# Kernel optimization log

Hardware: AMD Instinct MI355X
Metric: run time of the kernel (lower is better)

The kernel has to match this reference:

```python
import jax, jax.numpy as jnp
import numpy as np

N, D_IN, D_OUT = 8192, 1024, 1024

def setup_inputs() -> dict:
    key = jax.random.key(0)
    kx, kq, kk, kv = jax.random.split(key, 4)
    s = 1.0 / np.sqrt(D_IN)
    return {
        "x": jax.random.normal(kx, (N, D_IN), dtype=jnp.float32),
        "Wq": jax.random.uniform(kq, (D_OUT, D_IN), dtype=jnp.float32, minval=-s, maxval=s),
        "Wk": jax.random.uniform(kk, (D_OUT, D_IN), dtype=jnp.float32, minval=-s, maxval=s),
        "Wv": jax.random.uniform(kv, (D_OUT, D_IN), dtype=jnp.float32, minval=-s, maxval=s),
    }

def reference(x, Wq, Wk, Wv):
    # Linear layers: y = x @ W.T (no bias, qkv_bias=False)
    q = x @ Wq.T  # [N, d_out]
    k = x @ Wk.T
    v = x @ Wv.T
    scores = q @ k.T  # [N, N]
    weights = jax.nn.softmax(scores / jnp.sqrt(jnp.float32(k.shape[-1])), axis=-1)
    return weights @ v  # [N, d_out]
```

## Files before the change

### kernel.cpp

```cpp
#include <hip/hip_runtime.h>
#include <stdint.h>

typedef __bf16 bf16_t;
typedef __bf16 bf16x8 __attribute__((ext_vector_type(8)));
typedef float f32x4 __attribute__((ext_vector_type(4)));
typedef int i32x4 __attribute__((ext_vector_type(4)));
typedef int i32x8 __attribute__((ext_vector_type(8)));

typedef const __attribute__((address_space(1))) void gv_t;
typedef __attribute__((address_space(3))) void lv_t;


template <int LDK>
__device__ __forceinline__ void stage_half2(const bf16_t* g, bf16_t* lh,
                                            int wave, int lane) {
#pragma unroll
  for (int i = 0; i < 2; ++i) {
    const int ub = i * 8192 + wave * 1024;
    const int o = ub + lane * 16;
    const int row = o >> 7;
    const int kb = (o & 127) ^ ((row & 7) << 4);
    const char* src = (const char*)g + (size_t)row * (LDK * 2) + kb;
    __builtin_amdgcn_global_load_lds((gv_t*)src, (lv_t*)(lh + (ub >> 1)), 16, 0, 0);
  }
}

__device__ __forceinline__ bf16x8 ld_frag2(const bf16_t* h, int r, int s, int lane) {
  int byte = r * 128 + s * 64 + ((lane >> 4) << 4);
  byte ^= (r & 7) << 4;
  return *(const bf16x8*)((const char*)h + byte);
}

template <int NN, int KEXT, int LDK>
__global__ __launch_bounds__(512) void gemm8p(
    const bf16_t* __restrict__ A, const bf16_t* __restrict__ Bt,
    float* __restrict__ Cf0, bf16_t* __restrict__ Cf1b,
    const float* __restrict__ rvec) {
  __shared__ __align__(16) bf16_t L[2][4][8192];

  const int tid = threadIdx.x;
  const int wave = tid >> 6;
  const int lane = tid & 63;

  const int bid = blockIdx.x;
  const int x = bid & 7;
  const int j = bid >> 3;
  const int ks = j >> 4;
  const int tm = (x << 2) | (j & 3);
  const int tn = (j >> 2) & 3;

  const bf16_t* Ab = A + (size_t)tm * (256 * LDK) + (size_t)ks * KEXT;
  const bf16_t* Bb = Bt + (size_t)tn * (256 * LDK) + (size_t)ks * KEXT;

  const int wr64 = (wave >> 2) * 64;
  const int wc32 = (wave & 3) * 32;
  const int fr = lane & 15;
  constexpr int nt = KEXT >> 6;

  f32x4 acc00[4][2], acc01[4][2], acc10[4][2], acc11[4][2];
#pragma unroll
  for (int m = 0; m < 4; ++m)
#pragma unroll
    for (int n = 0; n < 2; ++n) {
      acc00[m][n] = (f32x4){0.f, 0.f, 0.f, 0.f};
      acc01[m][n] = (f32x4){0.f, 0.f, 0.f, 0.f};
      acc10[m][n] = (f32x4){0.f, 0.f, 0.f, 0.f};
      acc11[m][n] = (f32x4){0.f, 0.f, 0.f, 0.f};
    }

  stage_half2<LDK>(Ab, &L[0][0][0], wave, lane);
  stage_half2<LDK>(Ab + (size_t)128 * LDK, &L[0][1][0], wave, lane);
  stage_half2<LDK>(Bb, &L[0][2][0], wave, lane);
  stage_half2<LDK>(Bb + (size_t)128 * LDK, &L[0][3][0], wave, lane);
  stage_half2<LDK>(Ab + 64, &L[1][0][0], wave, lane);
  stage_half2<LDK>(Bb + 64, &L[1][2][0], wave, lane);
  stage_half2<LDK>(Bb + (size_t)128 * LDK + 64, &L[1][3][0], wave, lane);
  asm volatile("s_waitcnt vmcnt(6)" ::: "memory");
  __builtin_amdgcn_s_barrier();

  bf16x8 a[4][2], bA[2][2], bB[2][2];

#pragma unroll 1
  for (int t = 0; t < nt; ++t) {
    const int cur = t & 1;
    const bf16_t* A0h = &L[cur][0][0];
    const bf16_t* A1h = &L[cur][1][0];
    const bf16_t* B0h = &L[cur][2][0];
    const bf16_t* B1h = &L[cur][3][0];

#pragma unroll
    for (int m = 0; m < 4; ++m)
#pragma unroll
      for (int s = 0; s < 2; ++s)
        a[m][s] = ld_frag2(A0h, wr64 + m * 16 + fr, s, lane);
#pragma unroll
    for (int n = 0; n < 2; ++n)
#pragma unroll
      for (int s = 0; s < 2; ++s)
        bA[n][s] = ld_frag2(B0h, wc32 + n * 16 + fr, s, lane);
    if (t + 1 < nt)
      stage_half2<LDK>(Ab + (size_t)128 * LDK + (t + 1) * 64, &L[cur ^ 1][1][0],
                       wave, lane);
    __builtin_amdgcn_s_barrier();
    __builtin_amdgcn_s_setprio(1);
#pragma unroll
    for (int s = 0; s < 2; ++s)
#pragma unroll
      for (int m = 0; m < 4; ++m)
#pragma unroll
        for (int n = 0; n < 2; ++n)
          acc00[m][n] = __builtin_amdgcn_mfma_f32_16x16x32_bf16(a[m][s], bA[n][s],
                                                                acc00[m][n], 0, 0, 0);
    __builtin_amdgcn_s_setprio(0);
    __builtin_amdgcn_s_barrier();

#pragma unroll
    for (int n = 0; n < 2; ++n)
#pragma unroll
      for (int s = 0; s < 2; ++s)
        bB[n][s] = ld_frag2(B1h, wc32 + n * 16 + fr, s, lane);
    if (t + 2 < nt)
      stage_half2<LDK>(Ab + (t + 2) * 64, &L[cur][0][0], wave, lane);
    __builtin_amdgcn_s_barrier();
    __builtin_amdgcn_s_setprio(1);
#pragma unroll
    for (int s = 0; s < 2; ++s)
#pragma unroll
      for (int m = 0; m < 4; ++m)
#pragma unroll
        for (int n = 0; n < 2; ++n)
          acc01[m][n] = __builtin_amdgcn_mfma_f32_16x16x32_bf16(a[m][s], bB[n][s],
                                                                acc01[m][n], 0, 0, 0);
    __builtin_amdgcn_s_setprio(0);
    __builtin_amdgcn_s_barrier();

#pragma unroll
    for (int m = 0; m < 4; ++m)
#pragma unroll
      for (int s = 0; s < 2; ++s)
        a[m][s] = ld_frag2(A1h, wr64 + m * 16 + fr, s, lane);
    if (t + 2 < nt)
      stage_half2<LDK>(Bb + (t + 2) * 64, &L[cur][2][0], wave, lane);
    __builtin_amdgcn_s_barrier();
    __builtin_amdgcn_s_setprio(1);
#pragma unroll
    for (int s = 0; s < 2; ++s)
#pragma unroll
      for (int m = 0; m < 4; ++m)
#pragma unroll
        for (int n = 0; n < 2; ++n)
          acc11[m][n] = __builtin_amdgcn_mfma_f32_16x16x32_bf16(a[m][s], bB[n][s],
                                                                acc11[m][n], 0, 0, 0);
    __builtin_amdgcn_s_setprio(0);
    __builtin_amdgcn_s_barrier();

    if (t + 2 < nt)
      stage_half2<LDK>(Bb + (size_t)128 * LDK + (t + 2) * 64, &L[cur][3][0],
                       wave, lane);
    __builtin_amdgcn_s_barrier();
    __builtin_amdgcn_s_setprio(1);
#pragma unroll
    for (int s = 0; s < 2; ++s)
#pragma unroll
      for (int m = 0; m < 4; ++m)
#pragma unroll
        for (int n = 0; n < 2; ++n)
          acc10[m][n] = __builtin_amdgcn_mfma_f32_16x16x32_bf16(a[m][s], bA[n][s],
                                                                acc10[m][n], 0, 0, 0);
    __builtin_amdgcn_s_setprio(0);
    if (t + 2 < nt)
      asm volatile("s_waitcnt vmcnt(6)" ::: "memory");
    else
      asm volatile("s_waitcnt vmcnt(0)" ::: "memory");
    __builtin_amdgcn_s_barrier();
  }

  const int fro = (lane >> 4) * 4;
#define STORE_QUAD(ACC, QM, QN)                                                  \
  _Pragma("unroll") for (int m = 0; m < 4; ++m) {                                \
    _Pragma("unroll") for (int n = 0; n < 2; ++n) {                              \
      const int row = tm * 256 + QM * 128 + wr64 + m * 16 + fro;                 \
      const int col = tn * 256 + QN * 128 + wc32 + n * 16 + fr;                  \
      const float4 rv = *(const float4*)&rvec[row];                              \
      if (ks == 0) {                                                             \
        _Pragma("unroll") for (int jj = 0; jj < 4; ++jj)                         \
            Cf0[(size_t)(row + jj) * NN + col] =                                 \
                ACC[m][n][jj] * ((const float*)&rv)[jj];                         \
      } else {                                                                   \
        _Pragma("unroll") for (int jj = 0; jj < 4; ++jj)                         \
            Cf1b[(size_t)(row + jj) * NN + col] =                                \
                (bf16_t)(ACC[m][n][jj] * ((const float*)&rv)[jj]);               \
      }                                                                          \
    }                                                                            \
  }
  STORE_QUAD(acc00, 0, 0)
  STORE_QUAD(acc01, 0, 1)
  STORE_QUAD(acc10, 1, 0)
  STORE_QUAD(acc11, 1, 1)
#undef STORE_QUAD
}

template <int NN, int KEXT, int LDK>
__global__ __launch_bounds__(512) void gemm2p(
    const bf16_t* __restrict__ A, const bf16_t* __restrict__ Bt,
    uint8_t* __restrict__ qo, uint8_t* __restrict__ ko,
    bf16_t* __restrict__ vtb) {
  __shared__ __align__(16) bf16_t L[2][3][8192];

  const int tid = threadIdx.x;
  const int wave = tid >> 6;
  const int lane = tid & 63;

  const int bid = blockIdx.x;
  const int x = bid & 7;
  const int j = bid >> 3;
  const int tm = (x << 2) | (j & 3);
  const int tn = j >> 2;

  const bf16_t* Ab = A + (size_t)tm * (256 * LDK);
  const bf16_t* Bb = Bt + (size_t)tn * (128 * LDK);

  const int wr64 = (wave >> 2) * 64;
  const int wc32 = (wave & 3) * 32;
  const int fr = lane & 15;
  constexpr int nt = KEXT >> 6;

  f32x4 acc0[4][2], acc1[4][2];
#pragma unroll
  for (int m = 0; m < 4; ++m)
#pragma unroll
    for (int n = 0; n < 2; ++n) {
      acc0[m][n] = (f32x4){0.f, 0.f, 0.f, 0.f};
      acc1[m][n] = (f32x4){0.f, 0.f, 0.f, 0.f};
    }

  stage_half2<LDK>(Ab, &L[0][0][0], wave, lane);
  stage_half2<LDK>(Ab + (size_t)128 * LDK, &L[0][1][0], wave, lane);
  stage_half2<LDK>(Bb, &L[0][2][0], wave, lane);
  stage_half2<LDK>(Ab + 64, &L[1][0][0], wave, lane);
  stage_half2<LDK>(Bb + 64, &L[1][2][0], wave, lane);
  asm volatile("s_waitcnt vmcnt(4)" ::: "memory");
  __builtin_amdgcn_s_barrier();

  bf16x8 a[4][2], b[2][2];

#pragma unroll 1
  for (int t = 0; t < nt; ++t) {
    const int cur = t & 1;
    const bf16_t* A0h = &L[cur][0][0];
    const bf16_t* A1h = &L[cur][1][0];
    const bf16_t* Bh = &L[cur][2][0];

#pragma unroll
    for (int m = 0; m < 4; ++m)
#pragma unroll
      for (int s = 0; s < 2; ++s)
        a[m][s] = ld_frag2(A0h, wr64 + m * 16 + fr, s, lane);
#pragma unroll
    for (int n = 0; n < 2; ++n)
#pragma unroll
      for (int s = 0; s < 2; ++s)
        b[n][s] = ld_frag2(Bh, wc32 + n * 16 + fr, s, lane);
    if (t + 1 < nt)
      stage_half2<LDK>(Ab + (size_t)128 * LDK + (t + 1) * 64, &L[cur ^ 1][1][0],
                       wave, lane);
    __builtin_amdgcn_s_barrier();
    __builtin_amdgcn_s_setprio(1);
#pragma unroll
    for (int s = 0; s < 2; ++s)
#pragma unroll
      for (int m = 0; m < 4; ++m)
#pragma unroll
        for (int n = 0; n < 2; ++n)
          acc0[m][n] = __builtin_amdgcn_mfma_f32_16x16x32_bf16(a[m][s], b[n][s],
                                                               acc0[m][n], 0, 0, 0);
    __builtin_amdgcn_s_setprio(0);
    __builtin_amdgcn_s_barrier();

#pragma unroll
    for (int m = 0; m < 4; ++m)
#pragma unroll
      for (int s = 0; s < 2; ++s)
        a[m][s] = ld_frag2(A1h, wr64 + m * 16 + fr, s, lane);
    if (t + 2 < nt) {
      stage_half2<LDK>(Ab + (t + 2) * 64, &L[cur][0][0], wave, lane);
      stage_half2<LDK>(Bb + (t + 2) * 64, &L[cur][2][0], wave, lane);
    }
    __builtin_amdgcn_s_barrier();
    __builtin_amdgcn_s_setprio(1);
#pragma unroll
    for (int s = 0; s < 2; ++s)
#pragma unroll
      for (int m = 0; m < 4; ++m)
#pragma unroll
        for (int n = 0; n < 2; ++n)
          acc1[m][n] = __builtin_amdgcn_mfma_f32_16x16x32_bf16(a[m][s], b[n][s],
                                                               acc1[m][n], 0, 0, 0);
    __builtin_amdgcn_s_setprio(0);
    if (t + 2 < nt)
      asm volatile("s_waitcnt vmcnt(4)" ::: "memory");
    else
      asm volatile("s_waitcnt vmcnt(0)" ::: "memory");
    __builtin_amdgcn_s_barrier();
  }

  const int fro = (lane >> 4) * 4;
#define STORE_HALF(ACC, QM)                                                      \
  _Pragma("unroll") for (int m = 0; m < 4; ++m) {                                \
    _Pragma("unroll") for (int n = 0; n < 2; ++n) {                              \
      const int row = tm * 256 + QM * 128 + wr64 + m * 16 + fro;                 \
      const int col = tn * 128 + wc32 + n * 16 + fr;                             \
      if (col < 1024) {                                                          \
        _Pragma("unroll") for (int jj = 0; jj < 4; ++jj) {                       \
          int pk = __builtin_amdgcn_cvt_pk_fp8_f32(ACC[m][n][jj],                \
                                                   ACC[m][n][jj], 0, false);     \
          qo[(size_t)(row + jj) * 1024 + col] = (uint8_t)pk;                     \
        }                                                                        \
      } else if (col < 2048) {                                                   \
        _Pragma("unroll") for (int jj = 0; jj < 4; ++jj) {                       \
          int pk = __builtin_amdgcn_cvt_pk_fp8_f32(ACC[m][n][jj],                \
                                                   ACC[m][n][jj], 0, false);     \
          ko[(size_t)(row + jj) * 1024 + (col - 1024)] = (uint8_t)pk;            \
        }                                                                        \
      } else {                                                                   \
        union { bf16_t h[4]; uint2 u; } tpk;                                     \
        _Pragma("unroll") for (int jj = 0; jj < 4; ++jj)                         \
            tpk.h[jj] = (bf16_t)ACC[m][n][jj];                                   \
        *(uint2*)&vtb[(size_t)(col - 2048) * 8192 + row] = tpk.u;                \
      }                                                                          \
    }                                                                            \
  }
  STORE_HALF(acc0, 0)
  STORE_HALF(acc1, 1)
#undef STORE_HALF
}


__device__ __forceinline__ void stage_half8(const uint8_t* g, uint8_t* lh,
                                            int wave, int lane) {
#pragma unroll
  for (int i = 0; i < 2; ++i) {
    const int ub = i * 8192 + wave * 1024;
    const int o = ub + lane * 16;
    const int row = o >> 7;
    const int col = (o & 127) ^ ((row & 7) << 4);
    __builtin_amdgcn_global_load_lds((gv_t*)(g + (size_t)row * 1024 + col),
                                     (lv_t*)(lh + ub), 16, 0, 0);
  }
}

__device__ __forceinline__ i32x8 ld_frag8h(const uint8_t* h, int r, int lane) {
  const int sw = (r & 7) << 4;
  const int kg = (lane >> 4) * 32;
  const uint8_t* b = h + r * 128;
  i32x4 lo = *(const i32x4*)(b + (kg ^ sw));
  i32x4 hi = *(const i32x4*)(b + ((kg ^ sw) ^ 16));
  i32x8 v;
  v[0] = lo[0]; v[1] = lo[1]; v[2] = lo[2]; v[3] = lo[3];
  v[4] = hi[0]; v[5] = hi[1]; v[6] = hi[2]; v[7] = hi[3];
  return v;
}

__global__ __launch_bounds__(512) void scores8p(
    const uint8_t* __restrict__ qf, const uint8_t* __restrict__ kf,
    bf16_t* __restrict__ S, float* __restrict__ partial) {
  __shared__ __align__(16) uint8_t L[2][4][16384];

  const int tid = threadIdx.x;
  const int wave = tid >> 6;
  const int lane = tid & 63;

  const int bid = blockIdx.x;
  const int x = bid & 7;
  const int j = bid >> 3;
  const int tm = (x << 2) | (j & 3);
  const int tn = j >> 2;

  const uint8_t* Ab = qf + (size_t)tm * 256 * 1024;
  const uint8_t* Bb = kf + (size_t)tn * 256 * 1024;

  const int wr64 = (wave >> 2) * 64;
  const int wc32 = (wave & 3) * 32;
  const int fr = lane & 15;
  constexpr int nt = 8;

  f32x4 acc00[4][2], acc01[4][2], acc10[4][2], acc11[4][2];
#pragma unroll
  for (int m = 0; m < 4; ++m)
#pragma unroll
    for (int n = 0; n < 2; ++n) {
      acc00[m][n] = (f32x4){0.f, 0.f, 0.f, 0.f};
      acc01[m][n] = (f32x4){0.f, 0.f, 0.f, 0.f};
      acc10[m][n] = (f32x4){0.f, 0.f, 0.f, 0.f};
      acc11[m][n] = (f32x4){0.f, 0.f, 0.f, 0.f};
    }

  stage_half8(Ab, &L[0][0][0], wave, lane);
  stage_half8(Ab + (size_t)128 * 1024, &L[0][1][0], wave, lane);
  stage_half8(Bb, &L[0][2][0], wave, lane);
  stage_half8(Bb + (size_t)128 * 1024, &L[0][3][0], wave, lane);
  stage_half8(Ab + 128, &L[1][0][0], wave, lane);
  stage_half8(Bb + (size_t)128 * 1024 + 128, &L[1][3][0], wave, lane);
  asm volatile("s_waitcnt vmcnt(4)" ::: "memory");
  __builtin_amdgcn_s_barrier();

  i32x8 a[4], bA[2], bB[2];

#pragma unroll 1
  for (int t = 0; t < nt; ++t) {
    const int cur = t & 1;
    const uint8_t* A0h = &L[cur][0][0];
    const uint8_t* A1h = &L[cur][1][0];
    const uint8_t* B0h = &L[cur][2][0];
    const uint8_t* B1h = &L[cur][3][0];

#pragma unroll
    for (int m = 0; m < 4; ++m) a[m] = ld_frag8h(A0h, wr64 + m * 16 + fr, lane);
#pragma unroll
    for (int n = 0; n < 2; ++n) bA[n] = ld_frag8h(B0h, wc32 + n * 16 + fr, lane);
    if (t + 1 < nt)
      stage_half8(Ab + (size_t)128 * 1024 + (t + 1) * 128, &L[cur ^ 1][1][0],
                  wave, lane);
    __builtin_amdgcn_s_barrier();
    __builtin_amdgcn_s_setprio(1);
#pragma unroll
    for (int m = 0; m < 4; ++m)
#pragma unroll
      for (int n = 0; n < 2; ++n)
        acc00[m][n] = __builtin_amdgcn_mfma_scale_f32_16x16x128_f8f6f4(
            a[m], bA[n], acc00[m][n], 0, 0, 0, 0x7F7F7F7F, 0, 0x7F7F7F7F);
    __builtin_amdgcn_s_setprio(0);
    __builtin_amdgcn_s_barrier();

#pragma unroll
    for (int n = 0; n < 2; ++n) bB[n] = ld_frag8h(B1h, wc32 + n * 16 + fr, lane);
    if (t + 1 < nt)
      stage_half8(Bb + (t + 1) * 128, &L[cur ^ 1][2][0], wave, lane);
    __builtin_amdgcn_s_barrier();
    __builtin_amdgcn_s_setprio(1);
#pragma unroll
    for (int m = 0; m < 4; ++m)
#pragma unroll
      for (int n = 0; n < 2; ++n)
        acc01[m][n] = __builtin_amdgcn_mfma_scale_f32_16x16x128_f8f6f4(
            a[m], bB[n], acc01[m][n], 0, 0, 0, 0x7F7F7F7F, 0, 0x7F7F7F7F);
    __builtin_amdgcn_s_setprio(0);
    __builtin_amdgcn_s_barrier();

#pragma unroll
    for (int m = 0; m < 4; ++m) a[m] = ld_frag8h(A1h, wr64 + m * 16 + fr, lane);
    if (t + 2 < nt)
      stage_half8(Ab + (t + 2) * 128, &L[cur][0][0], wave, lane);
    __builtin_amdgcn_s_barrier();
    __builtin_amdgcn_s_setprio(1);
#pragma unroll
    for (int m = 0; m < 4; ++m)
#pragma unroll
      for (int n = 0; n < 2; ++n)
        acc11[m][n] = __builtin_amdgcn_mfma_scale_f32_16x16x128_f8f6f4(
            a[m], bB[n], acc11[m][n], 0, 0, 0, 0x7F7F7F7F, 0, 0x7F7F7F7F);
    __builtin_amdgcn_s_setprio(0);
    __builtin_amdgcn_s_barrier();

    if (t + 2 < nt)
      stage_half8(Bb + (size_t)128 * 1024 + (t + 2) * 128, &L[cur][3][0],
                  wave, lane);
    __builtin_amdgcn_s_barrier();
    __builtin_amdgcn_s_setprio(1);
#pragma unroll
    for (int m = 0; m < 4; ++m)
#pragma unroll
      for (int n = 0; n < 2; ++n)
        acc10[m][n] = __builtin_amdgcn_mfma_scale_f32_16x16x128_f8f6f4(
            a[m], bA[n], acc10[m][n], 0, 0, 0, 0x7F7F7F7F, 0, 0x7F7F7F7F);
    __builtin_amdgcn_s_setprio(0);
    if (t + 2 < nt)
      asm volatile("s_waitcnt vmcnt(4)" ::: "memory");
    else
      asm volatile("s_waitcnt vmcnt(0)" ::: "memory");
    __builtin_amdgcn_s_barrier();
  }

  const int fro = (lane >> 4) * 4;
#define EXPSTORE(ACC, QM, QN)                                                    \
  _Pragma("unroll") for (int m = 0; m < 4; ++m)                                  \
  _Pragma("unroll") for (int n = 0; n < 2; ++n)                                  \
  _Pragma("unroll") for (int jj = 0; jj < 4; ++jj) {                             \
    float e = __expf(ACC[m][n][jj]);                                             \
    ACC[m][n][jj] = e;                                                           \
    const int row = tm * 256 + QM * 128 + wr64 + m * 16 + fro + jj;              \
    const int col = tn * 256 + QN * 128 + wc32 + n * 16 + fr;                    \
    S[(size_t)row * 8192 + col] = (bf16_t)e;                                     \
  }
  EXPSTORE(acc00, 0, 0)
  EXPSTORE(acc01, 0, 1)
  EXPSTORE(acc10, 1, 0)
  EXPSTORE(acc11, 1, 1)
#undef EXPSTORE
  float* lsum = (float*)&L[0][0][0];
#define ROWSUM(A0, A1, QM)                                                       \
  _Pragma("unroll") for (int m = 0; m < 4; ++m) {                                \
    _Pragma("unroll") for (int jj = 0; jj < 4; ++jj) {                           \
      float s = A0[m][0][jj] + A0[m][1][jj] + A1[m][0][jj] + A1[m][1][jj];       \
      s += __shfl_xor(s, 1, 64);                                                 \
      s += __shfl_xor(s, 2, 64);                                                 \
      s += __shfl_xor(s, 4, 64);                                                 \
      s += __shfl_xor(s, 8, 64);                                                 \
      if (fr == 0) {                                                             \
        const int rl = QM * 128 + wr64 + m * 16 + fro + jj;                      \
        lsum[rl * 4 + (wave & 3)] = s;                                           \
      }                                                                          \
    }                                                                            \
  }
  ROWSUM(acc00, acc01, 0)
  ROWSUM(acc10, acc11, 1)
#undef ROWSUM
  __syncthreads();
  if (tid < 256) {
    float s = lsum[tid * 4] + lsum[tid * 4 + 1] + lsum[tid * 4 + 2] +
              lsum[tid * 4 + 3];
    partial[(size_t)tn * 8192 + tm * 256 + tid] = s;
  }
}

__global__ __launch_bounds__(256) void cvt_fused(const float* __restrict__ x,
                                                 const float* __restrict__ wq,
                                                 const float* __restrict__ wk,
                                                 const float* __restrict__ wv,
                                                 bf16_t* __restrict__ dst,
                                                 float sq) {
  constexpr int NX = 8192 * 1024 / 8;
  constexpr int NW = 1024 * 1024 / 8;
  const int i = blockIdx.x * 256 + threadIdx.x;
  const float* s;
  int k = i;
  float scale;
  if (i < NX) {
    s = x; scale = 1.0f;
  } else if (i < NX + NW) {
    s = wq; k = i - NX; scale = sq;
  } else if (i < NX + 2 * NW) {
    s = wk; k = i - NX - NW; scale = sq;
  } else {
    s = wv; k = i - NX - 2 * NW; scale = 1.0f;
  }
  const float4* sp = (const float4*)s + (size_t)k * 2;
  float4 x0 = sp[0], x1 = sp[1];
  bf16x8 o;
  o[0] = (bf16_t)(x0.x * scale);
  o[1] = (bf16_t)(x0.y * scale);
  o[2] = (bf16_t)(x0.z * scale);
  o[3] = (bf16_t)(x0.w * scale);
  o[4] = (bf16_t)(x1.x * scale);
  o[5] = (bf16_t)(x1.y * scale);
  o[6] = (bf16_t)(x1.z * scale);
  o[7] = (bf16_t)(x1.w * scale);
  ((bf16x8*)dst)[i] = o;
}

__global__ __launch_bounds__(256) void rowsum_recip(const float* __restrict__ partial,
                                                    float* __restrict__ r) {
  int row = blockIdx.x * 256 + threadIdx.x;
  float s = 0.f;
#pragma unroll
  for (int t = 0; t < 32; ++t) s += partial[(size_t)t * 8192 + row];
  r[row] = 1.0f / s;
}

__global__ __launch_bounds__(256) void add_p1(float* __restrict__ out,
                                              const bf16_t* __restrict__ p1b) {
  size_t i = (size_t)blockIdx.x * 256 + threadIdx.x;
  bf16x8 b = ((const bf16x8*)p1b)[i];
  float4 a0 = ((const float4*)out)[i * 2];
  float4 a1 = ((const float4*)out)[i * 2 + 1];
  a0.x += (float)b[0];
  a0.y += (float)b[1];
  a0.z += (float)b[2];
  a0.w += (float)b[3];
  a1.x += (float)b[4];
  a1.y += (float)b[5];
  a1.z += (float)b[6];
  a1.w += (float)b[7];
  ((float4*)out)[i * 2] = a0;
  ((float4*)out)[i * 2 + 1] = a1;
}

extern "C" void kernel_launch(void* const* d_in, const int* in_sizes, int n_in,
                              void* d_out, int out_size, void* d_ws, size_t ws_size,
                              hipStream_t stream) {
  const int N = 8192, D = 1024;
  const float* x = (const float*)d_in[0];
  const float* Wq = (const float*)d_in[1];
  const float* Wk = (const float*)d_in[2];
  const float* Wv = (const float*)d_in[3];
  float* out = (float*)d_out;

  uint8_t* qf = (uint8_t*)d_ws;
  uint8_t* kf = qf + (size_t)N * D;
  bf16_t* vt = (bf16_t*)(kf + (size_t)N * D);
  bf16_t* S = vt + (size_t)N * D;
  bf16_t* xb = S;
  bf16_t* P1b = (bf16_t*)d_ws;
  float* rvec = (float*)(S + (size_t)N * N);
  float* partial = out;

  const float sq = 0.1767766953f;

  const int ncv = (N * D + 3 * D * D) / 8;
  cvt_fused<<<ncv / 256, 256, 0, stream>>>(x, Wq, Wk, Wv, xb, sq);

  gemm2p<3072, 1024, 1024><<<(N / 256) * (3 * D / 128), 512, 0, stream>>>(
      xb, xb + (size_t)N * D, qf, kf, vt);

  scores8p<<<(N / 256) * (N / 256), 512, 0, stream>>>(qf, kf, S, partial);

  rowsum_recip<<<N / 256, 256, 0, stream>>>(partial, rvec);

  gemm8p<1024, 4096, 8192><<<(N / 256) * (D / 256) * 2, 512, 0, stream>>>(
      S, vt, out, P1b, rvec);

  add_p1<<<(N * D / 8) / 256, 256, 0, stream>>>(out, P1b);
}
```

Measured before the change: 302.5 us.

## Switch PV GEMM to 32x32 MFMA and fuse row-sum reciprocal into it

The P·V GEMM now uses 32x32x16 bf16 MFMA instructions with 16-wide accumulators in place of 16x16x32 tiles, which cuts the number of MFMA issues and LDS fragment loads per tile. Each block also sums the per-row softmax partials for its 256 rows into shared memory at kernel start, so the separate rowsum_recip launch is gone. The partials buffer moves from the output buffer to the workspace, because the GEMM writes the output while other blocks still read the partials. The cost is that every block redundantly recomputes the row sums, plus an extra sync before the main loop.

Result: slower. 317.5 us (+4.9%).

```diff
diff --git a/kernel.cpp b/kernel.cpp
--- a/kernel.cpp
+++ b/kernel.cpp
@@ -4,6 +4,7 @@
 typedef __bf16 bf16_t;
 typedef __bf16 bf16x8 __attribute__((ext_vector_type(8)));
 typedef float f32x4 __attribute__((ext_vector_type(4)));
+typedef float f32x16 __attribute__((ext_vector_type(16)));
 typedef int i32x4 __attribute__((ext_vector_type(4)));
 typedef int i32x8 __attribute__((ext_vector_type(8)));
 
@@ -31,12 +32,20 @@
   return *(const bf16x8*)((const char*)h + byte);
 }
 
+__device__ __forceinline__ bf16x8 ld_frag32(const bf16_t* h, int r, int ks,
+                                            int lane) {
+  int byte = r * 128 + ks * 32 + ((lane >> 5) << 4);
+  byte ^= (r & 7) << 4;
+  return *(const bf16x8*)((const char*)h + byte);
+}
+
 template <int NN, int KEXT, int LDK>
-__global__ __launch_bounds__(512) void gemm8p(
+__global__ __launch_bounds__(512) void gemm8p32(
     const bf16_t* __restrict__ A, const bf16_t* __restrict__ Bt,
     float* __restrict__ Cf0, bf16_t* __restrict__ Cf1b,
-    const float* __restrict__ rvec) {
+    const float* __restrict__ partial) {
   __shared__ __align__(16) bf16_t L[2][4][8192];
+  __shared__ float rl[256];
 
   const int tid = threadIdx.x;
   const int wave = tid >> 6;
@@ -49,24 +58,31 @@
   const int tm = (x << 2) | (j & 3);
   const int tn = (j >> 2) & 3;
 
+  if (tid < 256) {
+    float s = 0.f;
+#pragma unroll
+    for (int t = 0; t < 32; ++t) s += partial[(size_t)t * 8192 + tm * 256 + tid];
+    rl[tid] = 1.0f / s;
+  }
+  __syncthreads();
+
   const bf16_t* Ab = A + (size_t)tm * (256 * LDK) + (size_t)ks * KEXT;
   const bf16_t* Bb = Bt + (size_t)tn * (256 * LDK) + (size_t)ks * KEXT;
 
   const int wr64 = (wave >> 2) * 64;
   const int wc32 = (wave & 3) * 32;
-  const int fr = lane & 15;
   constexpr int nt = KEXT >> 6;
 
-  f32x4 acc00[4][2], acc01[4][2], acc10[4][2], acc11[4][2];
-#pragma unroll
-  for (int m = 0; m < 4; ++m)
-#pragma unroll
-    for (int n = 0; n < 2; ++n) {
-      acc00[m][n] = (f32x4){0.f, 0.f, 0.f, 0.f};
-      acc01[m][n] = (f32x4){0.f, 0.f, 0.f, 0.f};
-      acc10[m][n] = (f32x4){0.f, 0.f, 0.f, 0.f};
-      acc11[m][n] = (f32x4){0.f, 0.f, 0.f, 0.f};
-    }
+  const f32x16 zz = {0.f, 0.f, 0.f, 0.f, 0.f, 0.f, 0.f, 0.f,
+                     0.f, 0.f, 0.f, 0.f, 0.f, 0.f, 0.f, 0.f};
+  f32x16 acc00[2], acc01[2], acc10[2], acc11[2];
+#pragma unroll
+  for (int mb = 0; mb < 2; ++mb) {
+    acc00[mb] = zz;
+    acc01[mb] = zz;
+    acc10[mb] = zz;
+    acc11[mb] = zz;
+  }
 
   stage_half2<LDK>(Ab, &L[0][0][0], wave, lane);
   stage_half2<LDK>(Ab + (size_t)128 * LDK, &L[0][1][0], wave, lane);
@@ -78,7 +94,8 @@
   asm volatile("s_waitcnt vmcnt(6)" ::: "memory");
   __builtin_amdgcn_s_barrier();
 
-  bf16x8 a[4][2], bA[2][2], bB[2][2];
+  bf16x8 a[2][4], bA[4], bB[4];
+  const int ar = (lane & 31);
 
 #pragma unroll 1
   for (int t = 0; t < nt; ++t) {
@@ -89,68 +106,56 @@
     const bf16_t* B1h = &L[cur][3][0];
 
 #pragma unroll
-    for (int m = 0; m < 4; ++m)
-#pragma unroll
-      for (int s = 0; s < 2; ++s)
-        a[m][s] = ld_frag2(A0h, wr64 + m * 16 + fr, s, lane);
-#pragma unroll
-    for (int n = 0; n < 2; ++n)
-#pragma unroll
-      for (int s = 0; s < 2; ++s)
-        bA[n][s] = ld_frag2(B0h, wc32 + n * 16 + fr, s, lane);
+    for (int mb = 0; mb < 2; ++mb)
+#pragma unroll
+      for (int k = 0; k < 4; ++k)
+        a[mb][k] = ld_frag32(A0h, wr64 + mb * 32 + ar, k, lane);
+#pragma unroll
+    for (int k = 0; k < 4; ++k) bA[k] = ld_frag32(B0h, wc32 + ar, k, lane);
     if (t + 1 < nt)
       stage_half2<LDK>(Ab + (size_t)128 * LDK + (t + 1) * 64, &L[cur ^ 1][1][0],
                        wave, lane);
     __builtin_amdgcn_s_barrier();
     __builtin_amdgcn_s_setprio(1);
 #pragma unroll
-    for (int s = 0; s < 2; ++s)
-#pragma unroll
-      for (int m = 0; m < 4; ++m)
-#pragma unroll
-        for (int n = 0; n < 2; ++n)
-          acc00[m][n] = __builtin_amdgcn_mfma_f32_16x16x32_bf16(a[m][s], bA[n][s],
-                                                                acc00[m][n], 0, 0, 0);
-    __builtin_amdgcn_s_setprio(0);
-    __builtin_amdgcn_s_barrier();
-
-#pragma unroll
-    for (int n = 0; n < 2; ++n)
-#pragma unroll
-      for (int s = 0; s < 2; ++s)
-        bB[n][s] = ld_frag2(B1h, wc32 + n * 16 + fr, s, lane);
+    for (int k = 0; k < 4; ++k)
+#pragma unroll
+      for (int mb = 0; mb < 2; ++mb)
+        acc00[mb] = __builtin_amdgcn_mfma_f32_32x32x16_bf16(a[mb][k], bA[k],
+                                                            acc00[mb], 0, 0, 0);
+    __builtin_amdgcn_s_setprio(0);
+    __builtin_amdgcn_s_barrier();
+
+#pragma unroll
+    for (int k = 0; k < 4; ++k) bB[k] = ld_frag32(B1h, wc32 + ar, k, lane);
     if (t + 2 < nt)
       stage_half2<LDK>(Ab + (t + 2) * 64, &L[cur][0][0], wave, lane);
     __builtin_amdgcn_s_barrier();
     __builtin_amdgcn_s_setprio(1);
 #pragma unroll
-    for (int s = 0; s < 2; ++s)
-#pragma unroll
-      for (int m = 0; m < 4; ++m)
-#pragma unroll
-        for (int n = 0; n < 2; ++n)
-          acc01[m][n] = __builtin_amdgcn_mfma_f32_16x16x32_bf16(a[m][s], bB[n][s],
-                                                                acc01[m][n], 0, 0, 0);
-    __builtin_amdgcn_s_setprio(0);
-    __builtin_amdgcn_s_barrier();
-
-#pragma unroll
-    for (int m = 0; m < 4; ++m)
-#pragma unroll
-      for (int s = 0; s < 2; ++s)
-        a[m][s] = ld_frag2(A1h, wr64 + m * 16 + fr, s, lane);
+    for (int k = 0; k < 4; ++k)
+#pragma unroll
+      for (int mb = 0; mb < 2; ++mb)
+        acc01[mb] = __builtin_amdgcn_mfma_f32_32x32x16_bf16(a[mb][k], bB[k],
+                                                            acc01[mb], 0, 0, 0);
+    __builtin_amdgcn_s_setprio(0);
+    __builtin_amdgcn_s_barrier();
+
+#pragma unroll
+    for (int mb = 0; mb < 2; ++mb)
+#pragma unroll
+      for (int k = 0; k < 4; ++k)
+        a[mb][k] = ld_frag32(A1h, wr64 + mb * 32 + ar, k, lane);
     if (t + 2 < nt)
       stage_half2<LDK>(Bb + (t + 2) * 64, &L[cur][2][0], wave, lane);
     __builtin_amdgcn_s_barrier();
     __builtin_amdgcn_s_setprio(1);
 #pragma unroll
-    for (int s = 0; s < 2; ++s)
-#pragma unroll
-      for (int m = 0; m < 4; ++m)
-#pragma unroll
-        for (int n = 0; n < 2; ++n)
-          acc11[m][n] = __builtin_amdgcn_mfma_f32_16x16x32_bf16(a[m][s], bB[n][s],
-                                                                acc11[m][n], 0, 0, 0);
+    for (int k = 0; k < 4; ++k)
+#pragma unroll
+      for (int mb = 0; mb < 2; ++mb)
+        acc11[mb] = __builtin_amdgcn_mfma_f32_32x32x16_bf16(a[mb][k], bB[k],
+                                                            acc11[mb], 0, 0, 0);
     __builtin_amdgcn_s_setprio(0);
     __builtin_amdgcn_s_barrier();
 
@@ -160,13 +165,11 @@
     __builtin_amdgcn_s_barrier();
     __builtin_amdgcn_s_setprio(1);
 #pragma unroll
-    for (int s = 0; s < 2; ++s)
-#pragma unroll
-      for (int m = 0; m < 4; ++m)
-#pragma unroll
-        for (int n = 0; n < 2; ++n)
-          acc10[m][n] = __builtin_amdgcn_mfma_f32_16x16x32_bf16(a[m][s], bA[n][s],
-                                                                acc10[m][n], 0, 0, 0);
+    for (int k = 0; k < 4; ++k)
+#pragma unroll
+      for (int mb = 0; mb < 2; ++mb)
+        acc10[mb] = __builtin_amdgcn_mfma_f32_32x32x16_bf16(a[mb][k], bA[k],
+                                                            acc10[mb], 0, 0, 0);
     __builtin_amdgcn_s_setprio(0);
     if (t + 2 < nt)
       asm volatile("s_waitcnt vmcnt(6)" ::: "memory");
@@ -175,29 +178,29 @@
     __builtin_amdgcn_s_barrier();
   }
 
-  const int fro = (lane >> 4) * 4;
-#define STORE_QUAD(ACC, QM, QN)                                                  \
-  _Pragma("unroll") for (int m = 0; m < 4; ++m) {                                \
-    _Pragma("unroll") for (int n = 0; n < 2; ++n) {                              \
-      const int row = tm * 256 + QM * 128 + wr64 + m * 16 + fro;                 \
-      const int col = tn * 256 + QN * 128 + wc32 + n * 16 + fr;                  \
-      const float4 rv = *(const float4*)&rvec[row];                              \
-      if (ks == 0) {                                                             \
-        _Pragma("unroll") for (int jj = 0; jj < 4; ++jj)                         \
-            Cf0[(size_t)(row + jj) * NN + col] =                                 \
-                ACC[m][n][jj] * ((const float*)&rv)[jj];                         \
-      } else {                                                                   \
-        _Pragma("unroll") for (int jj = 0; jj < 4; ++jj)                         \
-            Cf1b[(size_t)(row + jj) * NN + col] =                                \
-                (bf16_t)(ACC[m][n][jj] * ((const float*)&rv)[jj]);               \
+  const int colb = tn * 256 + wc32 + (lane & 31);
+  const int rsub = (lane >> 5) << 2;
+#define STORE_QUAD32(ACC, QM, QN)                                                \
+  _Pragma("unroll") for (int mb = 0; mb < 2; ++mb) {                             \
+    _Pragma("unroll") for (int g = 0; g < 4; ++g) {                              \
+      const int lrow = QM * 128 + wr64 + mb * 32 + g * 8 + rsub;                 \
+      const int row = tm * 256 + lrow;                                           \
+      const int col = QN * 128 + colb;                                           \
+      const float4 rv = *(const float4*)&rl[lrow];                               \
+      _Pragma("unroll") for (int jj = 0; jj < 4; ++jj) {                         \
+        const float v = ACC[mb][g * 4 + jj] * ((const float*)&rv)[jj];           \
+        if (ks == 0)                                                             \
+          Cf0[(size_t)(row + jj) * NN + col] = v;                                \
+        else                                                                     \
+          Cf1b[(size_t)(row + jj) * NN + col] = (bf16_t)v;                       \
       }                                                                          \
     }                                                                            \
   }
-  STORE_QUAD(acc00, 0, 0)
-  STORE_QUAD(acc01, 0, 1)
-  STORE_QUAD(acc10, 1, 0)
-  STORE_QUAD(acc11, 1, 1)
-#undef STORE_QUAD
+  STORE_QUAD32(acc00, 0, 0)
+  STORE_QUAD32(acc01, 0, 1)
+  STORE_QUAD32(acc10, 1, 0)
+  STORE_QUAD32(acc11, 1, 1)
+#undef STORE_QUAD32
 }
 
 template <int NN, int KEXT, int LDK>
@@ -558,15 +561,6 @@
   ((bf16x8*)dst)[i] = o;
 }
 
-__global__ __launch_bounds__(256) void rowsum_recip(const float* __restrict__ partial,
-                                                    float* __restrict__ r) {
-  int row = blockIdx.x * 256 + threadIdx.x;
-  float s = 0.f;
-#pragma unroll
-  for (int t = 0; t < 32; ++t) s += partial[(size_t)t * 8192 + row];
-  r[row] = 1.0f / s;
-}
-
 __global__ __launch_bounds__(256) void add_p1(float* __restrict__ out,
                                               const bf16_t* __restrict__ p1b) {
   size_t i = (size_t)blockIdx.x * 256 + threadIdx.x;
@@ -601,8 +595,7 @@
   bf16_t* S = vt + (size_t)N * D;
   bf16_t* xb = S;
   bf16_t* P1b = (bf16_t*)d_ws;
-  float* rvec = (float*)(S + (size_t)N * N);
-  float* partial = out;
+  float* partial = (float*)(S + (size_t)N * N);
 
   const float sq = 0.1767766953f;
 
@@ -614,10 +607,8 @@
 
   scores8p<<<(N / 256) * (N / 256), 512, 0, stream>>>(qf, kf, S, partial);
 
-  rowsum_recip<<<N / 256, 256, 0, stream>>>(partial, rvec);
-
-  gemm8p<1024, 4096, 8192><<<(N / 256) * (D / 256) * 2, 512, 0, stream>>>(
-      S, vt, out, P1b, rvec);
+  gemm8p32<1024, 4096, 8192><<<(N / 256) * (D / 256) * 2, 512, 0, stream>>>(
+      S, vt, out, P1b, partial);
 
   add_p1<<<(N * D / 8) / 256, 256, 0, stream>>>(out, P1b);
 }
```
